# Performance work log

Hardware: AMD Instinct MI355X
Metric: run time of the kernel (lower is better)

Reference implementation:

```python
import jax, jax.numpy as jnp
import numpy as np

B, C, H = 8, 512, 2048
GROUPS = 32
EPS = 1e-6


def setup_inputs() -> dict:
    key = jax.random.key(0)
    ks = jax.random.split(key, 10)
    s = 1.0 / np.sqrt(C)
    return {
        "x": jax.random.normal(ks[0], (B, C, H), dtype=jnp.float32),
        "gamma": jnp.ones((C,), jnp.float32),
        "beta": jnp.zeros((C,), jnp.float32),
        "wq": jax.random.normal(ks[1], (C, C), jnp.float32) * s,
        "bq": jnp.zeros((C,), jnp.float32),
        "wk": jax.random.normal(ks[2], (C, C), jnp.float32) * s,
        "bk": jnp.zeros((C,), jnp.float32),
        "wv": jax.random.normal(ks[3], (C, C), jnp.float32) * s,
        "bv": jnp.zeros((C,), jnp.float32),
        "wp": jax.random.normal(ks[4], (C, C), jnp.float32) * s,
        "bp": jnp.zeros((C,), jnp.float32),
    }


def group_norm(x, gamma, beta):
    b, c, h = x.shape
    xr = x.reshape(b, GROUPS, c // GROUPS, h)
    mean = xr.mean(axis=(2, 3), keepdims=True)
    var = xr.var(axis=(2, 3), keepdims=True)
    xn = ((xr - mean) * jax.lax.rsqrt(var + EPS)).reshape(b, c, h)
    return xn * gamma[None, :, None] + beta[None, :, None]


def conv1x1(x, w, b):
    # 1x1 Conv1d == channel-mixing GEMM: [C_out,C_in] x [b,C_in,h]
    return jnp.einsum("oc,bch->boh", w, x) + b[None, :, None]


def reference(x, gamma, beta, wq, bq, wk, bk, wv, bv, wp, bp):
    b, c, h = x.shape
    hn = group_norm(x, gamma, beta)
    q = conv1x1(hn, wq, bq)  # [b,c,h]
    k = conv1x1(hn, wk, bk)
    v = conv1x1(hn, wv, bv)
    # scores w[b,i,j] = sum_c q[b,c,i] k[b,c,j] / sqrt(c)
    w = jnp.einsum("bci,bcj->bij", q, k) * (c ** -0.5)
    w = jax.nn.softmax(w, axis=2)
    # h_[b,c,i] = sum_j v[b,c,j] w[b,i,j]
    h_ = jnp.einsum("bcj,bij->bci", v, w)
    out = conv1x1(h_, wp, bp)
    return x + out
```

## Files before the change

kernel.cpp:

```cpp
#include <hip/hip_runtime.h>
#include <stdint.h>

typedef unsigned short u16;
typedef short s16x8 __attribute__((ext_vector_type(8)));
typedef float f32x4 __attribute__((ext_vector_type(4)));

#define BM 128
#define BN 128
#define BK 32
#define KPAD 40

__device__ __forceinline__ float bf2f(u16 b) {
    union { unsigned int u; float f; } v; v.u = ((unsigned int)b) << 16; return v.f;
}
__device__ __forceinline__ u16 f2bf(float f) {
    union { float f; unsigned int u; } v; v.f = f;
    unsigned int u = v.u;
    u += 0x7fffu + ((u >> 16) & 1u);
    return (u16)(u >> 16);
}
__device__ __forceinline__ void async_cp16(const u16* g, u16* l) {
    __builtin_amdgcn_global_load_lds((const __attribute__((address_space(1))) void*)g,
                                     (__attribute__((address_space(3))) void*)l, 16, 0, 0);
}

__global__ __launch_bounds__(256) void gn_stats(const float* __restrict__ x,
                                                float* __restrict__ mean,
                                                float* __restrict__ rstd) {
    const int bg = blockIdx.x;
    const float* p = x + (long)bg * 16 * 2048;
    float s = 0.f, ss = 0.f;
    for (int it = 0; it < 32; it++) {
        const float4 v = *reinterpret_cast<const float4*>(p + ((it * 256 + threadIdx.x) << 2));
        s += v.x + v.y + v.z + v.w;
        ss += v.x * v.x + v.y * v.y + v.z * v.z + v.w * v.w;
    }
    const int lane = threadIdx.x & 63, wave = threadIdx.x >> 6;
#pragma unroll
    for (int o = 32; o > 0; o >>= 1) { s += __shfl_down(s, o, 64); ss += __shfl_down(ss, o, 64); }
    __shared__ float rb[8];
    if (lane == 0) { rb[wave] = s; rb[4 + wave] = ss; }
    __syncthreads();
    if (threadIdx.x == 0) {
        float S = rb[0] + rb[1] + rb[2] + rb[3];
        float SS = rb[4] + rb[5] + rb[6] + rb[7];
        float mu = S * (1.f / 32768.f);
        float var = SS * (1.f / 32768.f) - mu * mu;
        mean[bg] = mu;
        rstd[bg] = rsqrtf(var + 1e-6f);
    }
}

__global__ __launch_bounds__(256) void gn_apply_t(const float* __restrict__ x,
                                                  const float* __restrict__ gamma,
                                                  const float* __restrict__ beta,
                                                  const float* __restrict__ mean,
                                                  const float* __restrict__ rstd,
                                                  u16* __restrict__ hnT) {
    const int b = blockIdx.z, c0 = blockIdx.y * 64, h0 = blockIdx.x * 64;
    __shared__ __align__(16) u16 T[64][72];
    const int tid = threadIdx.x;
#pragma unroll
    for (int sidx = 0; sidx < 4; sidx++) {
        int ch = tid + sidx * 256;
        int cc = ch >> 4, h4 = (ch & 15) * 4;
        int c = c0 + cc;
        float mu = mean[b * 32 + (c >> 4)], rs = rstd[b * 32 + (c >> 4)];
        float ga = gamma[c], be = beta[c];
        const float4 v = *reinterpret_cast<const float4*>(x + ((long)b * 512 + c) * 2048 + h0 + h4);
        ushort4 pk;
        pk.x = f2bf((v.x - mu) * rs * ga + be);
        pk.y = f2bf((v.y - mu) * rs * ga + be);
        pk.z = f2bf((v.z - mu) * rs * ga + be);
        pk.w = f2bf((v.w - mu) * rs * ga + be);
        *reinterpret_cast<ushort4*>(&T[cc][h4]) = pk;
    }
    __syncthreads();
#pragma unroll
    for (int sidx = 0; sidx < 2; sidx++) {
        int ch = tid + sidx * 256;
        int hh = ch >> 3, c8 = (ch & 7) * 8;
        unsigned int o[4];
#pragma unroll
        for (int i = 0; i < 4; i++) {
            u16 lo = T[c8 + 2 * i][hh];
            u16 hi = T[c8 + 2 * i + 1][hh];
            o[i] = (unsigned int)lo | ((unsigned int)hi << 16);
        }
        *reinterpret_cast<uint4*>(hnT + ((long)b * 2048 + h0 + hh) * 512 + c0 + c8) =
            uint4{o[0], o[1], o[2], o[3]};
    }
}

__global__ __launch_bounds__(256) void w2bf(const float* __restrict__ a,
                                            const float* __restrict__ b,
                                            const float* __restrict__ c,
                                            u16* __restrict__ dst) {
    const float* s = (blockIdx.y == 0) ? a : (blockIdx.y == 1) ? b : c;
    const int i = (blockIdx.x * 256 + threadIdx.x) * 4;
    const float4 v = *reinterpret_cast<const float4*>(s + i);
    ushort4 p;
    p.x = f2bf(v.x); p.y = f2bf(v.y); p.z = f2bf(v.z); p.w = f2bf(v.w);
    *reinterpret_cast<ushort4*>(dst + (long)blockIdx.y * 262144 + i) = p;
}

__global__ __launch_bounds__(256) void softmax_rows(u16* __restrict__ S) {
    u16* p = S + (long)blockIdx.x * 2048;
    const int tid = threadIdx.x;
    uint4 v = *reinterpret_cast<const uint4*>(p + (tid << 3));
    unsigned int w[4] = {v.x, v.y, v.z, v.w};
    float f[8];
#pragma unroll
    for (int i = 0; i < 4; i++) {
        f[2 * i]     = bf2f((u16)(w[i] & 0xffffu));
        f[2 * i + 1] = bf2f((u16)(w[i] >> 16));
    }
    float m = f[0];
#pragma unroll
    for (int i = 1; i < 8; i++) m = fmaxf(m, f[i]);
    const int lane = tid & 63, wave = tid >> 6;
#pragma unroll
    for (int o = 32; o > 0; o >>= 1) m = fmaxf(m, __shfl_down(m, o, 64));
    __shared__ float rb[4];
    __shared__ float bc;
    if (lane == 0) rb[wave] = m;
    __syncthreads();
    if (tid == 0) bc = fmaxf(fmaxf(rb[0], rb[1]), fmaxf(rb[2], rb[3]));
    __syncthreads();
    m = bc;
    float s = 0.f;
#pragma unroll
    for (int i = 0; i < 8; i++) { f[i] = __expf(f[i] - m); s += f[i]; }
#pragma unroll
    for (int o = 32; o > 0; o >>= 1) s += __shfl_down(s, o, 64);
    __syncthreads();
    if (lane == 0) rb[wave] = s;
    __syncthreads();
    if (tid == 0) bc = 1.f / (rb[0] + rb[1] + rb[2] + rb[3]);
    __syncthreads();
    const float inv = bc;
#pragma unroll
    for (int i = 0; i < 4; i++)
        w[i] = (unsigned int)f2bf(f[2 * i] * inv) | ((unsigned int)f2bf(f[2 * i + 1] * inv) << 16);
    *reinterpret_cast<uint4*>(p + (tid << 3)) = uint4{w[0], w[1], w[2], w[3]};
}

template <int EPI>
__global__ __launch_bounds__(256) void gemm_tn_a(const u16* __restrict__ Ag, long sA,
                                                 const u16* __restrict__ Bg, long sB,
                                                 const float* __restrict__ bias,
                                                 const float* __restrict__ Xg, long sX,
                                                 void* __restrict__ Ogv, long sO,
                                                 int K, int lda, int ldb, int ldo,
                                                 float scale) {
    const int b = blockIdx.z;
    Ag += (long)b * sA;
    Bg += (long)b * sB;
    const int m0 = blockIdx.y * BM;
    const int n0 = blockIdx.x * BN;

    __shared__ __align__(16) u16 As[2][BM * BK];
    __shared__ __align__(16) u16 Bs[2][BN * BK];

    const int tid = threadIdx.x;
    const int wave = tid >> 6;
    const int lane = tid & 63;
    const int quad = lane >> 4;
    const int l16 = lane & 15;
    const int wm = (wave >> 1) * 64;
    const int wn = (wave & 1) * 64;
    const int rl = lane >> 2;
    const int cl = (lane & 3) * 8;

    f32x4 acc[4][4];
#pragma unroll
    for (int i = 0; i < 4; i++)
#pragma unroll
        for (int j = 0; j < 4; j++) acc[i][j] = f32x4{0.f, 0.f, 0.f, 0.f};

    auto stage = [&](int buf, int k0) {
#pragma unroll
        for (int j = 0; j < 2; j++) {
            const int rbase = wave * 32 + j * 16;
            async_cp16(Ag + (long)(m0 + rbase + rl) * lda + k0 + cl, &As[buf][rbase * BK]);
            async_cp16(Bg + (long)(n0 + rbase + rl) * ldb + k0 + cl, &Bs[buf][rbase * BK]);
        }
    };
    auto compute = [&](int buf) {
        s16x8 af[4], bfr[4];
#pragma unroll
        for (int i = 0; i < 4; i++)
            af[i] = *reinterpret_cast<const s16x8*>(&As[buf][(wm + i * 16 + l16) * BK + quad * 8]);
#pragma unroll
        for (int j = 0; j < 4; j++)
            bfr[j] = *reinterpret_cast<const s16x8*>(&Bs[buf][(wn + j * 16 + l16) * BK + quad * 8]);
#pragma unroll
        for (int i = 0; i < 4; i++)
#pragma unroll
            for (int j = 0; j < 4; j++)
                acc[i][j] = __builtin_amdgcn_mfma_f32_16x16x32_bf16(af[i], bfr[j], acc[i][j], 0, 0, 0);
    };

    stage(0, 0);
    for (int k0 = 0; k0 < K; k0 += 2 * BK) {
        __syncthreads();
        stage(1, k0 + BK);
        compute(0);
        __syncthreads();
        if (k0 + 2 * BK < K) stage(0, k0 + 2 * BK);
        compute(1);
    }

#pragma unroll
    for (int i = 0; i < 4; i++) {
        const int mb = m0 + wm + i * 16 + quad * 4;
#pragma unroll
        for (int j = 0; j < 4; j++) {
            const int n = n0 + wn + j * 16 + l16;
            if (EPI == 0) {
                u16* O = (u16*)Ogv + (long)b * sO;
#pragma unroll
                for (int r = 0; r < 4; r++) {
                    float vv = acc[i][j][r] * scale;
                    if (bias) vv += bias[mb + r];
                    O[(long)(mb + r) * ldo + n] = f2bf(vv);
                }
            } else if (EPI == 1) {
                u16* O = (u16*)Ogv + (long)b * sO;
                ushort4 pk;
                pk.x = f2bf(acc[i][j][0] + bias[mb + 0]);
                pk.y = f2bf(acc[i][j][1] + bias[mb + 1]);
                pk.z = f2bf(acc[i][j][2] + bias[mb + 2]);
                pk.w = f2bf(acc[i][j][3] + bias[mb + 3]);
                *reinterpret_cast<ushort4*>(&O[(long)n * ldo + mb]) = pk;
            } else {
                float* O = (float*)Ogv + (long)b * sO;
                const float* X = Xg + (long)b * sX;
                const float bn = bias[n];
                const float4 xv = *reinterpret_cast<const float4*>(&X[(long)n * ldo + mb]);
                float4 pk;
                pk.x = acc[i][j][0] + bn + xv.x;
                pk.y = acc[i][j][1] + bn + xv.y;
                pk.z = acc[i][j][2] + bn + xv.z;
                pk.w = acc[i][j][3] + bn + xv.w;
                *reinterpret_cast<float4*>(&O[(long)n * ldo + mb]) = pk;
            }
        }
    }
}

__global__ __launch_bounds__(256) void qkv_a(const u16* __restrict__ wb3,
                                             const u16* __restrict__ hnT,
                                             const float* __restrict__ bq,
                                             const float* __restrict__ bk,
                                             const float* __restrict__ bv,
                                             u16* __restrict__ qT, u16* __restrict__ kT,
                                             u16* __restrict__ vv) {
    const long HC = 1048576;
    const int z = blockIdx.z;
    const int which = z % 3, b = z / 3;
    const u16* Ag = wb3 + which * 262144;
    const u16* Bg = hnT + (long)b * HC;
    const int m0 = blockIdx.y * BM;
    const int n0 = blockIdx.x * BN;

    __shared__ __align__(16) u16 As[2][BM * BK];
    __shared__ __align__(16) u16 Bs[2][BN * BK];

    const int tid = threadIdx.x;
    const int wave = tid >> 6;
    const int lane = tid & 63;
    const int quad = lane >> 4;
    const int l16 = lane & 15;
    const int wm = (wave >> 1) * 64;
    const int wn = (wave & 1) * 64;
    const int rl = lane >> 2;
    const int cl = (lane & 3) * 8;

    f32x4 acc[4][4];
#pragma unroll
    for (int i = 0; i < 4; i++)
#pragma unroll
        for (int j = 0; j < 4; j++) acc[i][j] = f32x4{0.f, 0.f, 0.f, 0.f};

    auto stage = [&](int buf, int k0) {
#pragma unroll
        for (int j = 0; j < 2; j++) {
            const int rbase = wave * 32 + j * 16;
            async_cp16(Ag + (long)(m0 + rbase + rl) * 512 + k0 + cl, &As[buf][rbase * BK]);
            async_cp16(Bg + (long)(n0 + rbase + rl) * 512 + k0 + cl, &Bs[buf][rbase * BK]);
        }
    };
    auto compute = [&](int buf) {
        s16x8 af[4], bfr[4];
#pragma unroll
        for (int i = 0; i < 4; i++)
            af[i] = *reinterpret_cast<const s16x8*>(&As[buf][(wm + i * 16 + l16) * BK + quad * 8]);
#pragma unroll
        for (int j = 0; j < 4; j++)
            bfr[j] = *reinterpret_cast<const s16x8*>(&Bs[buf][(wn + j * 16 + l16) * BK + quad * 8]);
#pragma unroll
        for (int i = 0; i < 4; i++)
#pragma unroll
            for (int j = 0; j < 4; j++)
                acc[i][j] = __builtin_amdgcn_mfma_f32_16x16x32_bf16(af[i], bfr[j], acc[i][j], 0, 0, 0);
    };

    stage(0, 0);
    for (int k0 = 0; k0 < 512; k0 += 2 * BK) {
        __syncthreads();
        stage(1, k0 + BK);
        compute(0);
        __syncthreads();
        if (k0 + 2 * BK < 512) stage(0, k0 + 2 * BK);
        compute(1);
    }

    if (which == 2) {
        u16* O = vv + (long)b * HC;
#pragma unroll
        for (int i = 0; i < 4; i++) {
            const int mb = m0 + wm + i * 16 + quad * 4;
#pragma unroll
            for (int j = 0; j < 4; j++) {
                const int n = n0 + wn + j * 16 + l16;
#pragma unroll
                for (int r = 0; r < 4; r++)
                    O[(long)(mb + r) * 2048 + n] = f2bf(acc[i][j][r] + bv[mb + r]);
            }
        }
    } else {
        const float* bias = which ? bk : bq;
        u16* O = (which ? kT : qT) + (long)b * HC;
#pragma unroll
        for (int i = 0; i < 4; i++) {
            const int mb = m0 + wm + i * 16 + quad * 4;
#pragma unroll
            for (int j = 0; j < 4; j++) {
                const int n = n0 + wn + j * 16 + l16;
                ushort4 pk;
                pk.x = f2bf(acc[i][j][0] + bias[mb + 0]);
                pk.y = f2bf(acc[i][j][1] + bias[mb + 1]);
                pk.z = f2bf(acc[i][j][2] + bias[mb + 2]);
                pk.w = f2bf(acc[i][j][3] + bias[mb + 3]);
                *reinterpret_cast<ushort4*>(&O[(long)n * 512 + mb]) = pk;
            }
        }
    }
}

template <int F32>
__device__ __forceinline__ void stage_tile(const char* G, int ld, int r0, int k0,
                                           u16* __restrict__ lds, int tid) {
    if (F32) {
        const float* g = (const float*)G;
#pragma unroll
        for (int s = 0; s < 4; s++) {
            const int c = tid + s * 256;
            const int row = c >> 3, col = (c & 7) * 4;
            const float4 v = *reinterpret_cast<const float4*>(g + (long)(r0 + row) * ld + k0 + col);
            ushort4 pk;
            pk.x = f2bf(v.x); pk.y = f2bf(v.y); pk.z = f2bf(v.z); pk.w = f2bf(v.w);
            *reinterpret_cast<ushort4*>(&lds[row * KPAD + col]) = pk;
        }
    } else {
        const u16* g = (const u16*)G;
#pragma unroll
        for (int s = 0; s < 2; s++) {
            const int c = tid + s * 256;
            const int row = c >> 2, col = (c & 3) * 8;
            const uint4 v = *reinterpret_cast<const uint4*>(g + (long)(r0 + row) * ld + k0 + col);
            *reinterpret_cast<uint4*>(&lds[row * KPAD + col]) = v;
        }
    }
}

template <int EPI, int AF32, int BF32>
__global__ __launch_bounds__(256) void gemm_tn(const void* __restrict__ Agv, long sA,
                                               const void* __restrict__ Bgv, long sB,
                                               const float* __restrict__ bias,
                                               const float* __restrict__ Xg, long sX,
                                               void* __restrict__ Ogv, long sO,
                                               int K, int lda, int ldb, int ldo,
                                               float scale) {
    const int b = blockIdx.z;
    const char* A8 = (const char*)Agv + (long)b * sA * (AF32 ? 4 : 2);
    const char* B8 = (const char*)Bgv + (long)b * sB * (BF32 ? 4 : 2);
    const int m0 = blockIdx.y * BM;
    const int n0 = blockIdx.x * BN;

    __shared__ __align__(16) u16 As[BM * KPAD];
    __shared__ __align__(16) u16 Bs[BN * KPAD];

    const int tid = threadIdx.x;
    const int wave = tid >> 6;
    const int lane = tid & 63;
    const int quad = lane >> 4;
    const int l16 = lane & 15;
    const int wm = (wave >> 1) * 64;
    const int wn = (wave & 1) * 64;

    f32x4 acc[4][4];
#pragma unroll
    for (int i = 0; i < 4; i++)
#pragma unroll
        for (int j = 0; j < 4; j++) acc[i][j] = f32x4{0.f, 0.f, 0.f, 0.f};

    for (int k0 = 0; k0 < K; k0 += BK) {
        __syncthreads();
        stage_tile<AF32>(A8, lda, m0, k0, As, tid);
        stage_tile<BF32>(B8, ldb, n0, k0, Bs, tid);
        __syncthreads();
        s16x8 af[4], bfr[4];
#pragma unroll
        for (int i = 0; i < 4; i++)
            af[i] = *reinterpret_cast<const s16x8*>(&As[(wm + i * 16 + l16) * KPAD + quad * 8]);
#pragma unroll
        for (int j = 0; j < 4; j++)
            bfr[j] = *reinterpret_cast<const s16x8*>(&Bs[(wn + j * 16 + l16) * KPAD + quad * 8]);
#pragma unroll
        for (int i = 0; i < 4; i++)
#pragma unroll
            for (int j = 0; j < 4; j++)
                acc[i][j] = __builtin_amdgcn_mfma_f32_16x16x32_bf16(af[i], bfr[j], acc[i][j], 0, 0, 0);
    }

#pragma unroll
    for (int i = 0; i < 4; i++) {
        const int mb = m0 + wm + i * 16 + quad * 4;
#pragma unroll
        for (int j = 0; j < 4; j++) {
            const int n = n0 + wn + j * 16 + l16;
            if (EPI == 0) {
                u16* O = (u16*)Ogv + (long)b * sO;
#pragma unroll
                for (int r = 0; r < 4; r++) {
                    float vv = acc[i][j][r] * scale;
                    if (bias) vv += bias[mb + r];
                    O[(long)(mb + r) * ldo + n] = f2bf(vv);
                }
            } else if (EPI == 1) {
                u16* O = (u16*)Ogv + (long)b * sO;
                ushort4 pk;
                pk.x = f2bf(acc[i][j][0] + bias[mb + 0]);
                pk.y = f2bf(acc[i][j][1] + bias[mb + 1]);
                pk.z = f2bf(acc[i][j][2] + bias[mb + 2]);
                pk.w = f2bf(acc[i][j][3] + bias[mb + 3]);
                *reinterpret_cast<ushort4*>(&O[(long)n * ldo + mb]) = pk;
            } else {
                float* O = (float*)Ogv + (long)b * sO;
                const float* X = Xg + (long)b * sX;
                const float bn = bias[n];
                const float4 xv = *reinterpret_cast<const float4*>(&X[(long)n * ldo + mb]);
                float4 pk;
                pk.x = acc[i][j][0] + bn + xv.x;
                pk.y = acc[i][j][1] + bn + xv.y;
                pk.z = acc[i][j][2] + bn + xv.z;
                pk.w = acc[i][j][3] + bn + xv.w;
                *reinterpret_cast<float4*>(&O[(long)n * ldo + mb]) = pk;
            }
        }
    }
}

extern "C" void kernel_launch(void* const* d_in, const int* in_sizes, int n_in,
                              void* d_out, int out_size, void* d_ws, size_t ws_size,
                              hipStream_t stream) {
    const float* x     = (const float*)d_in[0];
    const float* gamma = (const float*)d_in[1];
    const float* beta  = (const float*)d_in[2];
    const float* wq    = (const float*)d_in[3];
    const float* bq    = (const float*)d_in[4];
    const float* wk    = (const float*)d_in[5];
    const float* bk    = (const float*)d_in[6];
    const float* wv    = (const float*)d_in[7];
    const float* bv    = (const float*)d_in[8];
    const float* wp    = (const float*)d_in[9];
    const float* bp    = (const float*)d_in[10];
    float* out = (float*)d_out;

    const long HC = (long)2048 * 512;
    const long HH = (long)2048 * 2048;
    const long WSZ = 512 * 512;
    const float scl = 0.044194173824159216f;

    char* ws = (char*)d_ws;
    float* meanb = (float*)ws;
    float* rstdb = (float*)(ws + 1024);
    u16* base = (u16*)(ws + 4096);

    const size_t FULL_NEED   = 4096 + 2 * (size_t)(24 * HC + 8 * HH);
    const size_t MED_NEED    = 4096 + 2 * (size_t)(32 * HC + HH);
    const size_t SMALL_NEED  = 4096 + 2 * (size_t)(4 * HC + HH);
    const size_t CHUNK512    = 4096 + 2 * (size_t)(4 * HC + 512 * 2048);

    gn_stats<<<256, 256, 0, stream>>>(x, meanb, rstdb);

    if (ws_size >= FULL_NEED) {
        u16* qT  = base;
        u16* kT  = qT + 8 * HC;
        u16* vv  = kT + 8 * HC;
        u16* Sb  = vv + 8 * HC;
        u16* hnT = Sb;
        u16* wb3 = Sb + 8 * HH - 3 * WSZ;
        u16* hT  = qT;
        u16* wpb = vv;

        w2bf<<<dim3(256, 3), 256, 0, stream>>>(wq, wk, wv, wb3);
        gn_apply_t<<<dim3(32, 8, 8), 256, 0, stream>>>(x, gamma, beta, meanb, rstdb, hnT);
        qkv_a<<<dim3(16, 4, 24), 256, 0, stream>>>(wb3, hnT, bq, bk, bv, qT, kT, vv);
        gemm_tn_a<0><<<dim3(16, 16, 8), 256, 0, stream>>>(qT, HC, kT, HC, nullptr, nullptr, 0,
                                                          Sb, HH, 512, 512, 512, 2048, scl);
        softmax_rows<<<16384, 256, 0, stream>>>(Sb);
        gemm_tn_a<0><<<dim3(4, 16, 8), 256, 0, stream>>>(Sb, HH, vv, HC, nullptr, nullptr, 0,
                                                         hT, HC, 2048, 2048, 2048, 512, 1.f);
        w2bf<<<dim3(256, 1), 256, 0, stream>>>(wp, wp, wp, wpb);
        gemm_tn_a<2><<<dim3(4, 16, 8), 256, 0, stream>>>(hT, HC, wpb, 0, bp, x, HC,
                                                         out, HC, 512, 512, 512, 2048, 1.f);
    } else if (ws_size >= MED_NEED) {
        u16* hnT = base;
        u16* qT  = hnT + 8 * HC;
        u16* kT  = qT + 8 * HC;
        u16* vv  = kT + 8 * HC;
        u16* Sb  = vv + 8 * HC;
        u16* hT  = hnT;
        gn_apply_t<<<dim3(32, 8, 8), 256, 0, stream>>>(x, gamma, beta, meanb, rstdb, hnT);
        gemm_tn<1, 1, 0><<<dim3(16, 4, 8), 256, 0, stream>>>(wq, 0, hnT, HC, bq, nullptr, 0,
                                                             qT, HC, 512, 512, 512, 512, 1.f);
        gemm_tn<1, 1, 0><<<dim3(16, 4, 8), 256, 0, stream>>>(wk, 0, hnT, HC, bk, nullptr, 0,
                                                             kT, HC, 512, 512, 512, 512, 1.f);
        gemm_tn<0, 1, 0><<<dim3(16, 4, 8), 256, 0, stream>>>(wv, 0, hnT, HC, bv, nullptr, 0,
                                                             vv, HC, 512, 512, 512, 2048, 1.f);
        for (int b = 0; b < 8; b++) {
            gemm_tn<0, 0, 0><<<dim3(16, 16, 1), 256, 0, stream>>>(qT + b * HC, 0, kT + b * HC, 0,
                                                                  nullptr, nullptr, 0, Sb, 0,
                                                                  512, 512, 512, 2048, scl);
            softmax_rows<<<2048, 256, 0, stream>>>(Sb);
            gemm_tn<0, 0, 0><<<dim3(4, 16, 1), 256, 0, stream>>>(Sb, 0, vv + b * HC, 0,
                                                                 nullptr, nullptr, 0, hT + b * HC, 0,
                                                                 2048, 2048, 2048, 512, 1.f);
        }
        gemm_tn<2, 0, 1><<<dim3(4, 16, 8), 256, 0, stream>>>(hT, HC, wp, 0, bp, x, HC,
                                                             out, HC, 512, 512, 512, 2048, 1.f);
    } else {
        const int CH = (ws_size >= SMALL_NEED) ? 2048 : ((ws_size >= CHUNK512) ? 512 : 128);
        u16* hn = base;
        u16* q  = hn + HC;
        u16* k  = q + HC;
        u16* v  = k + HC;
        u16* Sc = v + HC;
        u16* hT = hn;
        for (int b = 0; b < 8; b++) {
            const float* xb = x + (long)b * HC;
            gn_apply_t<<<dim3(32, 8, 1), 256, 0, stream>>>(xb, gamma, beta,
                                                           meanb + b * 32, rstdb + b * 32, hn);
            gemm_tn<1, 1, 0><<<dim3(16, 4, 1), 256, 0, stream>>>(wq, 0, hn, 0, bq, nullptr, 0,
                                                                 q, 0, 512, 512, 512, 512, 1.f);
            gemm_tn<1, 1, 0><<<dim3(16, 4, 1), 256, 0, stream>>>(wk, 0, hn, 0, bk, nullptr, 0,
                                                                 k, 0, 512, 512, 512, 512, 1.f);
            gemm_tn<0, 1, 0><<<dim3(16, 4, 1), 256, 0, stream>>>(wv, 0, hn, 0, bv, nullptr, 0,
                                                                 v, 0, 512, 512, 512, 2048, 1.f);
            for (int i0 = 0; i0 < 2048; i0 += CH) {
                gemm_tn<0, 0, 0><<<dim3(16, CH / 128, 1), 256, 0, stream>>>(
                    q + (long)i0 * 512, 0, k, 0, nullptr, nullptr, 0, Sc, 0,
                    512, 512, 512, 2048, scl);
                softmax_rows<<<CH, 256, 0, stream>>>(Sc);
                gemm_tn<0, 0, 0><<<dim3(4, CH / 128, 1), 256, 0, stream>>>(
                    Sc, 0, v, 0, nullptr, nullptr, 0, hT + (long)i0 * 512, 0,
                    2048, 2048, 2048, 512, 1.f);
            }
            gemm_tn<2, 0, 1><<<dim3(4, 16, 1), 256, 0, stream>>>(hT, 0, wp, 0, bp, xb, 0,
                                                                 out + (long)b * HC, 0,
                                                                 512, 512, 512, 2048, 1.f);
        }
    }
}
```

Before: 325.3 us.

## Fuse softmax normalization into PV GEMM A-tile load with separate row stats

After: 347.9 us. +6.9%, slower.

```diff
diff --git a/kernel.cpp b/kernel.cpp
--- a/kernel.cpp
+++ b/kernel.cpp
@@ -143,6 +143,145 @@
     for (int i = 0; i < 4; i++)
         w[i] = (unsigned int)f2bf(f[2 * i] * inv) | ((unsigned int)f2bf(f[2 * i + 1] * inv) << 16);
     *reinterpret_cast<uint4*>(p + (tid << 3)) = uint4{w[0], w[1], w[2], w[3]};
+}
+
+__global__ __launch_bounds__(256) void row_stats(const u16* __restrict__ S,
+                                                 float* __restrict__ mrow,
+                                                 float* __restrict__ linv) {
+    const int r = blockIdx.x * 4 + (threadIdx.x >> 6);
+    const int lane = threadIdx.x & 63;
+    const u16* p = S + (long)r * 2048;
+    float f[32];
+#pragma unroll
+    for (int seg = 0; seg < 4; seg++) {
+        const uint4 v = *reinterpret_cast<const uint4*>(p + seg * 512 + lane * 8);
+        const unsigned int w[4] = {v.x, v.y, v.z, v.w};
+#pragma unroll
+        for (int i = 0; i < 4; i++) {
+            f[seg * 8 + 2 * i]     = bf2f((u16)(w[i] & 0xffffu));
+            f[seg * 8 + 2 * i + 1] = bf2f((u16)(w[i] >> 16));
+        }
+    }
+    float m = f[0];
+#pragma unroll
+    for (int i = 1; i < 32; i++) m = fmaxf(m, f[i]);
+#pragma unroll
+    for (int o = 32; o > 0; o >>= 1) m = fmaxf(m, __shfl_down(m, o, 64));
+    m = __shfl(m, 0, 64);
+    float s = 0.f;
+#pragma unroll
+    for (int i = 0; i < 32; i++) s += __expf(f[i] - m);
+#pragma unroll
+    for (int o = 32; o > 0; o >>= 1) s += __shfl_down(s, o, 64);
+    if (lane == 0) { mrow[r] = m; linv[r] = 1.f / s; }
+}
+
+__global__ __launch_bounds__(256) void pv_fused(const u16* __restrict__ S,
+                                                const u16* __restrict__ vv,
+                                                const float* __restrict__ mrow,
+                                                const float* __restrict__ linv,
+                                                u16* __restrict__ hT) {
+    const long HH = 4194304, HC = 1048576;
+    const int b = blockIdx.z;
+    const u16* A = S + (long)b * HH;
+    const u16* B = vv + (long)b * HC;
+    u16* O = hT + (long)b * HC;
+    const int m0 = blockIdx.y * 64;
+    const int n0 = blockIdx.x * 128;
+
+    __shared__ __align__(16) u16 As[2][64 * 32];
+    __shared__ __align__(16) u16 Bs[2][128 * 32];
+    __shared__ float ms[64], ls[64];
+
+    const int tid = threadIdx.x;
+    const int wave = tid >> 6;
+    const int lane = tid & 63;
+    const int quad = lane >> 4;
+    const int l16 = lane & 15;
+    const int wm = (wave >> 1) * 32;
+    const int wn = (wave & 1) * 64;
+    const int rl = lane >> 2;
+    const int cl = (lane & 3) * 8;
+    const int ar = tid >> 2;
+    const int ac = (tid & 3) * 8;
+
+    if (tid < 64) {
+        ms[tid] = mrow[b * 2048 + m0 + tid];
+        ls[tid] = linv[b * 2048 + m0 + tid];
+    }
+
+    f32x4 acc[2][4];
+#pragma unroll
+    for (int i = 0; i < 2; i++)
+#pragma unroll
+        for (int j = 0; j < 4; j++) acc[i][j] = f32x4{0.f, 0.f, 0.f, 0.f};
+
+    auto load_a = [&](int k0) -> uint4 {
+        return *reinterpret_cast<const uint4*>(A + (long)(m0 + ar) * 2048 + k0 + ac);
+    };
+    auto finish_a = [&](int buf, uint4 v) {
+        const float mm = ms[ar];
+        const float li = ls[ar];
+        const unsigned int w[4] = {v.x, v.y, v.z, v.w};
+        unsigned int o[4];
+#pragma unroll
+        for (int i = 0; i < 4; i++) {
+            float a = __expf(bf2f((u16)(w[i] & 0xffffu)) - mm) * li;
+            float d = __expf(bf2f((u16)(w[i] >> 16)) - mm) * li;
+            o[i] = (unsigned int)f2bf(a) | ((unsigned int)f2bf(d) << 16);
+        }
+        *reinterpret_cast<uint4*>(&As[buf][ar * 32 + ac]) = uint4{o[0], o[1], o[2], o[3]};
+    };
+    auto stage_b = [&](int buf, int k0) {
+#pragma unroll
+        for (int j = 0; j < 2; j++) {
+            const int rbase = wave * 32 + j * 16;
+            async_cp16(B + (long)(n0 + rbase + rl) * 2048 + k0 + cl, &Bs[buf][rbase * 32]);
+        }
+    };
+    auto compute = [&](int buf) {
+        s16x8 af[2], bf4[4];
+#pragma unroll
+        for (int i = 0; i < 2; i++)
+            af[i] = *reinterpret_cast<const s16x8*>(&As[buf][(wm + i * 16 + l16) * 32 + quad * 8]);
+#pragma unroll
+        for (int j = 0; j < 4; j++)
+            bf4[j] = *reinterpret_cast<const s16x8*>(&Bs[buf][(wn + j * 16 + l16) * 32 + quad * 8]);
+#pragma unroll
+        for (int i = 0; i < 2; i++)
+#pragma unroll
+            for (int j = 0; j < 4; j++)
+                acc[i][j] = __builtin_amdgcn_mfma_f32_16x16x32_bf16(af[i], bf4[j], acc[i][j], 0, 0, 0);
+    };
+
+    uint4 av = load_a(0);
+    stage_b(0, 0);
+    __syncthreads();
+    finish_a(0, av);
+
+    for (int k0 = 0; k0 < 2048; k0 += 64) {
+        uint4 av1 = load_a(k0 + 32);
+        __syncthreads();
+        stage_b(1, k0 + 32);
+        compute(0);
+        finish_a(1, av1);
+        __syncthreads();
+        if (k0 + 64 < 2048) { av = load_a(k0 + 64); stage_b(0, k0 + 64); }
+        compute(1);
+        if (k0 + 64 < 2048) finish_a(0, av);
+    }
+
+#pragma unroll
+    for (int i = 0; i < 2; i++) {
+        const int mb = m0 + wm + i * 16 + quad * 4;
+#pragma unroll
+        for (int j = 0; j < 4; j++) {
+            const int n = n0 + wn + j * 16 + l16;
+#pragma unroll
+            for (int r = 0; r < 4; r++)
+                O[(long)(mb + r) * 512 + n] = f2bf(acc[i][j][r]);
+        }
+    }
 }
 
 template <int EPI>
@@ -505,15 +644,16 @@
         u16* wb3 = Sb + 8 * HH - 3 * WSZ;
         u16* hT  = qT;
         u16* wpb = vv;
+        float* mrow = (float*)kT;
+        float* linv = mrow + 16384;
 
         w2bf<<<dim3(256, 3), 256, 0, stream>>>(wq, wk, wv, wb3);
         gn_apply_t<<<dim3(32, 8, 8), 256, 0, stream>>>(x, gamma, beta, meanb, rstdb, hnT);
         qkv_a<<<dim3(16, 4, 24), 256, 0, stream>>>(wb3, hnT, bq, bk, bv, qT, kT, vv);
         gemm_tn_a<0><<<dim3(16, 16, 8), 256, 0, stream>>>(qT, HC, kT, HC, nullptr, nullptr, 0,
                                                           Sb, HH, 512, 512, 512, 2048, scl);
-        softmax_rows<<<16384, 256, 0, stream>>>(Sb);
-        gemm_tn_a<0><<<dim3(4, 16, 8), 256, 0, stream>>>(Sb, HH, vv, HC, nullptr, nullptr, 0,
-                                                         hT, HC, 2048, 2048, 2048, 512, 1.f);
+        row_stats<<<4096, 256, 0, stream>>>(Sb, mrow, linv);
+        pv_fused<<<dim3(4, 32, 8), 256, 0, stream>>>(Sb, vv, mrow, linv, hT);
         w2bf<<<dim3(256, 1), 256, 0, stream>>>(wp, wp, wp, wpb);
         gemm_tn_a<2><<<dim3(4, 16, 8), 256, 0, stream>>>(hT, HC, wpb, 0, bp, x, HC,
                                                          out, HC, 512, 512, 512, 2048, 1.f);
```
